# Performance work log

Hardware: AMD Instinct MI355X
Metric: run time of the kernel (lower is better)

Reference implementation:

```python
import jax, jax.numpy as jnp
import numpy as np

N, T, C, H, W = 4, 8, 512, 14, 14
HEADS = 8
D = C // HEADS            # 64 per-head dim
S = T * H * W             # 1568 sequence length
EPS = 1e-8
NEG = -2.0**32 + 1.0      # padding value used by the original module


def setup_inputs() -> dict:
    key = jax.random.key(0)
    ks = jax.random.split(key, 8)
    shp = (N, T, C, H, W)
    scale = 1.0 / np.sqrt(C)
    return {
        "queries": jax.random.normal(ks[0], shp, jnp.float32),
        "keys": jax.random.normal(ks[1], shp, jnp.float32),
        "values": jax.random.normal(ks[2], shp, jnp.float32),
        "Wq": jax.random.normal(ks[3], (C, C), jnp.float32) * scale,
        "bq": jnp.zeros((C,), jnp.float32),
        "Wk": jax.random.normal(ks[4], (C, C), jnp.float32) * scale,
        "bk": jnp.zeros((C,), jnp.float32),
        "Wv": jax.random.normal(ks[5], (C, C), jnp.float32) * scale,
        "bv": jnp.zeros((C,), jnp.float32),
        "gamma": jnp.ones((C,), jnp.float32),
        "beta": jnp.zeros((C,), jnp.float32),
    }


def _proj(x, Wt, b):
    # 1x1 Conv2d + ReLU over channel dim of (N, T, C, H, W)
    y = jnp.einsum('ntchw,oc->ntohw', x, Wt) + b[None, None, :, None, None]
    return jax.nn.relu(y)


def _flatten(x):
    # (N, T, C, H, W) -> (N, T*H*W, C)
    return x.transpose(0, 1, 3, 4, 2).reshape(N, S, C)


def _split_heads(x):
    # torch.cat(torch.chunk(x, HEADS, dim=2), dim=0): (N, S, C) -> (HEADS*N, S, D)
    return x.reshape(N, S, HEADS, D).transpose(2, 0, 1, 3).reshape(HEADS * N, S, D)


def reference(queries, keys, values, Wq, bq, Wk, bk, Wv, bv, gamma, beta):
    Qf = _flatten(_proj(queries, Wq, bq))
    Kf = _flatten(_proj(keys, Wk, bk))
    Vf = _flatten(_proj(values, Wv, bv))
    q_flat = _flatten(queries)   # residual + query mask source
    k_flat = _flatten(keys)      # key mask source

    Q_ = _split_heads(Qf)
    K_ = _split_heads(Kf)
    V_ = _split_heads(Vf)

    scores = jnp.einsum('bqd,bkd->bqk', Q_, K_) / jnp.sqrt(jnp.float32(D))

    # key padding mask: sign(|sum over C|), tiled over heads -> (HEADS*N, 1, S)
    key_mask = jnp.sign(jnp.abs(k_flat.sum(-1)))          # (N, S)
    km = jnp.tile(key_mask, (HEADS, 1))[:, None, :]
    scores = jnp.where(km == 0.0, NEG, scores)

    attn = jax.nn.softmax(scores, axis=-1)

    # query padding mask (multiplicative) -> (HEADS*N, S, 1)
    query_mask = jnp.sign(jnp.abs(q_flat.sum(-1)))        # (N, S)
    qm = jnp.tile(query_mask, (HEADS, 1))[:, :, None]
    attn = attn * qm

    out = jnp.einsum('bqk,bkd->bqd', attn, V_)
    # merge heads back: inverse of _split_heads
    out = out.reshape(HEADS, N, S, D).transpose(1, 2, 0, 3).reshape(N, S, C)

    out = out + q_flat  # residual

    # custom LayerNorm: torch .std() is unbiased (ddof=1)
    mean = out.mean(-1, keepdims=True)
    std = jnp.sqrt(out.var(-1, ddof=1, keepdims=True))
    out = gamma * (out - mean) / (std + EPS) + beta

    # reshape back to (N, T, C, H, W)
    return out.reshape(N, T, H, W, C).transpose(0, 1, 4, 2, 3)
```

## Files before the change

kernel.cpp:

```cpp
#include <hip/hip_runtime.h>
#include <math.h>

#define N_ 4
#define T_ 8
#define C_ 512
#define H_ 14
#define W_ 14
#define HEADS_ 8
#define D_ 64
#define HW_ 196
#define S_ 1568
#define P_TOT 6272
#define KMP_ 1600
#define NEGL_ (-1.0e38f)
#define EPS_ 1e-8f
#define QSC_ 0.18033688011112042f

typedef __attribute__((ext_vector_type(8))) short short8v;
typedef __attribute__((ext_vector_type(4))) float float4v;
typedef __attribute__((ext_vector_type(4))) unsigned short ushort4v;
typedef unsigned short ushort_t;

__device__ __forceinline__ ushort_t f2bf(float f) {
    union { float f; unsigned u; } a; a.f = f;
    unsigned r = (a.u + 0x7FFFu + ((a.u >> 16) & 1u)) >> 16;
    return (ushort_t)r;
}
__device__ __forceinline__ float bf2f(ushort_t u) {
    union { unsigned u; float f; } t; t.u = ((unsigned)u) << 16; return t.f;
}
__device__ __forceinline__ unsigned cvt_pk_bf16(float lo, float hi) {
    unsigned r;
    asm("v_cvt_pk_bf16_f32 %0, %1, %2" : "=v"(r) : "v"(lo), "v"(hi));
    return r;
}
__device__ __forceinline__ float exp2_fast(float x) {
    float r;
    asm("v_exp_f32 %0, %1" : "=v"(r) : "v"(x));
    return r;
}
__device__ __forceinline__ float max3f(float a, float b, float c) {
    float r;
    asm("v_max3_f32 %0, %1, %2, %3" : "=v"(r) : "v"(a), "v"(b), "v"(c));
    return r;
}
__device__ __forceinline__ float4v mfma16(short8v a, short8v b, float4v c) {
    return __builtin_amdgcn_mfma_f32_16x16x32_bf16(a, b, c, 0, 0, 0);
}
__device__ __forceinline__ void gload_lds16(const void* g, void* l) {
    __builtin_amdgcn_global_load_lds(
        (const __attribute__((address_space(1))) unsigned int*)g,
        (__attribute__((address_space(3))) unsigned int*)l,
        16, 0, 0);
}
__device__ __forceinline__ void gload_lds4(const void* g, void* l) {
    __builtin_amdgcn_global_load_lds(
        (const __attribute__((address_space(1))) unsigned int*)g,
        (__attribute__((address_space(3))) unsigned int*)l,
        4, 0, 0);
}

__global__ __launch_bounds__(256) void transpose_kernel(
    const float* __restrict__ q_in, const float* __restrict__ k_in,
    const float* __restrict__ v_in, ushort_t* __restrict__ qbf,
    ushort_t* __restrict__ kbf, ushort_t* __restrict__ vbf,
    const float* __restrict__ Wq, const float* __restrict__ Wk,
    const float* __restrict__ Wv, ushort_t* __restrict__ Wbf)
{
    __shared__ float Xs[64][197];
    const int z = blockIdx.z;
    const int nt = blockIdx.x;
    const int ct = blockIdx.y;
    const int tid = threadIdx.x;

    if (z == 3) {
        const int blk = nt * 8 + ct;
        #pragma unroll
        for (int i = 0; i < 3; ++i) {
            const int q = (blk * 3 + i) * 256 + tid;
            const int zi = q >> 16;
            const int qi = q & 65535;
            const float* src = (zi == 0) ? Wq : (zi == 1) ? Wk : Wv;
            const float4 v = *(const float4*)(src + qi * 4);
            ushort4v pk;
            pk[0] = f2bf(v.x); pk[1] = f2bf(v.y);
            pk[2] = f2bf(v.z); pk[3] = f2bf(v.w);
            *(ushort4v*)(Wbf + (long)zi * 262144 + qi * 4) = pk;
        }
        return;
    }

    const float* src = (z == 0) ? q_in : (z == 1) ? k_in : v_in;
    ushort_t* dst = (z == 0) ? qbf : (z == 1) ? kbf : vbf;

    const long gbase = ((long)nt * C_ + ct * 64) * HW_;
    #pragma unroll
    for (int i = 0; i < 13; ++i) {
        const int idx = i * 256 + tid;
        if (idx < 3136) {
            const int c = idx / 49;
            const int q4 = idx - c * 49;
            const float4 v = *(const float4*)(src + gbase + c * HW_ + q4 * 4);
            Xs[c][q4 * 4 + 0] = v.x;
            Xs[c][q4 * 4 + 1] = v.y;
            Xs[c][q4 * 4 + 2] = v.z;
            Xs[c][q4 * 4 + 3] = v.w;
        }
    }
    __syncthreads();
    const long pbase = (long)nt * HW_;
    const int c0 = (tid & 15) * 4;
    #pragma unroll
    for (int i = 0; i < 13; ++i) {
        const int idx = i * 256 + tid;
        if (idx < 3136) {
            const int hw = idx >> 4;
            ushort4v pk;
            #pragma unroll
            for (int e = 0; e < 4; ++e) pk[e] = f2bf(Xs[c0 + e][hw]);
            *(ushort4v*)(dst + (pbase + hw) * C_ + ct * 64 + c0) = pk;
        }
    }
}

__global__ __launch_bounds__(256) void mask_kernel(
    const ushort_t* __restrict__ qbf, const ushort_t* __restrict__ kbf,
    float* __restrict__ qm, float* __restrict__ km)
{
    const int tid = threadIdx.x;
    const int w = tid >> 6, lane = tid & 63;
    const int p = blockIdx.x * 4 + w;
    const short8v qv = *(const short8v*)(qbf + (long)p * C_ + lane * 8);
    const short8v kv = *(const short8v*)(kbf + (long)p * C_ + lane * 8);
    float sq = 0.f, sk = 0.f;
    #pragma unroll
    for (int j = 0; j < 8; ++j) {
        sq += bf2f(((const ushort_t*)&qv)[j]);
        sk += bf2f(((const ushort_t*)&kv)[j]);
    }
    #pragma unroll
    for (int off = 32; off > 0; off >>= 1) {
        sq += __shfl_xor(sq, off, 64);
        sk += __shfl_xor(sk, off, 64);
    }
    if (lane == 0) {
        const int n = p / S_, s = p - n * S_;
        qm[p] = (sq != 0.f) ? 1.f : 0.f;
        km[n * KMP_ + s] = (sk != 0.f) ? 0.f : NEGL_;
    }
    if (blockIdx.x == 0 && tid < 128) {
        const int nn = tid >> 5;
        const int ss = S_ + (tid & 31);
        km[nn * KMP_ + ss] = NEGL_;
    }
}

__global__ __launch_bounds__(256) void proj_all(
    const ushort_t* __restrict__ qbf, const ushort_t* __restrict__ kbf,
    const ushort_t* __restrict__ vbf, const ushort_t* __restrict__ Wbf,
    const float* __restrict__ bq, const float* __restrict__ bk,
    const float* __restrict__ bv,
    ushort_t* __restrict__ Qh, ushort_t* __restrict__ Kh,
    ushort_t* __restrict__ Vt)
{
    __shared__ char lds[49152];

    const int fid = blockIdx.x;
    const int xcd = fid & 7;
    const int iin = fid >> 3;
    const int v = xcd * 147 + iin;
    const int z = v / 392;
    const int rem = v - z * 392;
    const int ptile = rem >> 3;
    const int head = rem & 7;

    const ushort_t* Xbf = (z == 0) ? qbf : (z == 1) ? kbf : vbf;
    const ushort_t* Wz = Wbf + (long)z * 262144;
    const float* bias = (z == 0) ? bq : (z == 1) ? bk : bv;
    ushort_t* outp = (z == 0) ? Qh : (z == 1) ? Kh : Vt;
    const bool TR = (z == 2);
    const float osc = (z == 0) ? QSC_ : 1.0f;

    const int tid = threadIdx.x;
    const int w = tid >> 6, lane = tid & 63, lg = lane >> 4, lo = lane & 15;
    const int wr = w >> 1, wc = w & 1;
    const int p0 = ptile * 128;
    const int o0 = head * 64;

    const int wbase = (tid & 192) * 16;

    float4v acc[2][4];
    #pragma unroll
    for (int a = 0; a < 2; ++a)
        #pragma unroll
        for (int b = 0; b < 4; ++b) acc[a][b] = (float4v){0.f, 0.f, 0.f, 0.f};

    auto stage = [&](int buf, int k0) {
        char* Xl = lds + buf * 24576;
        char* Wl = Xl + 16384;
        #pragma unroll
        for (int i = 0; i < 4; ++i) {
            const int sl = tid + i * 256;
            const int row = sl >> 3, sir = sl & 7;
            const int c16 = sir ^ (row & 7);
            gload_lds16(Xbf + (long)(p0 + row) * C_ + k0 + c16 * 8,
                        Xl + i * 4096 + wbase);
        }
        #pragma unroll
        for (int i = 0; i < 2; ++i) {
            const int sl = tid + i * 256;
            const int row = sl >> 3, sir = sl & 7;
            const int c16 = sir ^ (row & 7);
            gload_lds16(Wz + (long)(o0 + row) * C_ + k0 + c16 * 8,
                        Wl + i * 4096 + wbase);
        }
    };

    stage(0, 0);
    #pragma unroll
    for (int kstep = 0; kstep < 8; ++kstep) {
        __syncthreads();
        if (kstep < 7) stage((kstep + 1) & 1, (kstep + 1) * 64);

        const char* Xl = lds + (kstep & 1) * 24576;
        const char* Wl = Xl + 16384;
        short8v wf[2][2], xf[4][2];
        #pragma unroll
        for (int a = 0; a < 2; ++a) {
            const int row = wc * 32 + a * 16 + lo;
            const int swr = (row & 7) << 4;
            #pragma unroll
            for (int ks = 0; ks < 2; ++ks) {
                const int base = row * 128 + ks * 64 + lg * 8;
                ((uint2*)&wf[a][ks])[0] = *(const uint2*)(Wl + (base ^ swr));
                ((uint2*)&wf[a][ks])[1] = *(const uint2*)(Wl + ((base + 32) ^ swr));
            }
        }
        #pragma unroll
        for (int b = 0; b < 4; ++b) {
            const int row = wr * 64 + b * 16 + lo;
            const int swr = (row & 7) << 4;
            #pragma unroll
            for (int ks = 0; ks < 2; ++ks) {
                const int base = row * 128 + ks * 64 + lg * 8;
                ((uint2*)&xf[b][ks])[0] = *(const uint2*)(Xl + (base ^ swr));
                ((uint2*)&xf[b][ks])[1] = *(const uint2*)(Xl + ((base + 32) ^ swr));
            }
        }
        __builtin_amdgcn_s_setprio(1);
        if (!TR) {
            #pragma unroll
            for (int ks = 0; ks < 2; ++ks)
                #pragma unroll
                for (int a = 0; a < 2; ++a)
                    #pragma unroll
                    for (int b = 0; b < 4; ++b)
                        acc[a][b] = mfma16(wf[a][ks], xf[b][ks], acc[a][b]);
        } else {
            #pragma unroll
            for (int ks = 0; ks < 2; ++ks)
                #pragma unroll
                for (int a = 0; a < 2; ++a)
                    #pragma unroll
                    for (int b = 0; b < 4; ++b)
                        acc[a][b] = mfma16(xf[b][ks], wf[a][ks], acc[a][b]);
        }
        __builtin_amdgcn_s_setprio(0);
    }

    if (!TR) {
        #pragma unroll
        for (int b = 0; b < 4; ++b) {
            const int p = p0 + wr * 64 + b * 16 + lo;
            const int nb = p / S_;
            const int s = p - nb * S_;
            #pragma unroll
            for (int a = 0; a < 2; ++a) {
                const int d0 = wc * 32 + a * 16 + lg * 4;
                const float4v bs = *(const float4v*)(bias + o0 + d0);
                ushort4v pk;
                #pragma unroll
                for (int e = 0; e < 4; ++e) {
                    float vv = acc[a][b][e] + bs[e];
                    vv = vv > 0.f ? vv : 0.f;
                    pk[e] = f2bf(vv * osc);
                }
                *(ushort4v*)(outp + ((long)(head * N_ + nb) * S_ + s) * D_ + d0) = pk;
            }
        }
    } else {
        #pragma unroll
        for (int a = 0; a < 2; ++a) {
            const int d = wc * 32 + a * 16 + lo;
            const float bsc = bias[o0 + d];
            #pragma unroll
            for (int b = 0; b < 4; ++b) {
                const int pb = p0 + wr * 64 + b * 16 + lg * 4;
                const int nb = pb / S_;
                const int s0 = pb - nb * S_;
                ushort4v pk;
                #pragma unroll
                for (int e = 0; e < 4; ++e) {
                    float vv = acc[a][b][e] + bsc;
                    vv = vv > 0.f ? vv : 0.f;
                    pk[e] = f2bf(vv);
                }
                *(ushort4v*)(outp + ((long)(head * N_ + nb) * D_ + d) * S_ + s0) = pk;
            }
        }
    }
}

__global__ __launch_bounds__(256) void attn_kernel(
    const ushort_t* __restrict__ Qh, const ushort_t* __restrict__ Kh,
    const ushort_t* __restrict__ Vt, const float* __restrict__ km,
    ushort_t* __restrict__ Pc, float* __restrict__ Ml)
{
    __shared__ char lds[16384 + 256];

    const int tid = threadIdx.x;
    const int lane = tid & 63;
    const int w = tid >> 6;
    const int lg = lane >> 4;
    const int lo = lane & 15;

    const int split = blockIdx.y;
    const int t1 = 7 + split * 6;
    const int t0 = split ? (1 + split * 6) : 0;

    const int fid = blockIdx.x;
    const int x = fid & 7;
    const int j = fid >> 3;
    const int b = x + 8 * (j / 25);
    const int q0 = (j % 25) * 64;
    const int n = b & (N_ - 1);

    char* Kl = lds;
    char* Vl = lds + 8192;
    const float* kms = (const float*)(lds + 16384);
    const int wbase = (tid & 192) * 16;

    const int qrow = q0 + w * 16 + lo;
    const int qcl = qrow < S_ ? qrow : S_ - 1;
    const ushort_t* qp = Qh + ((long)b * S_ + qcl) * D_ + lg * 4;
    short8v qf[2];
    #pragma unroll
    for (int ks = 0; ks < 2; ++ks) {
        ((uint2*)&qf[ks])[0] = *(const uint2*)(qp + ks * 32);
        ((uint2*)&qf[ks])[1] = *(const uint2*)(qp + ks * 32 + 16);
    }

    float4v acc[4];
    #pragma unroll
    for (int dt = 0; dt < 4; ++dt) acc[dt] = (float4v){0.f, 0.f, 0.f, 0.f};
    float m_run = -INFINITY, l_run = 0.f;

    auto stage = [&](int kb) {
        #pragma unroll
        for (int i = 0; i < 2; ++i) {
            const int s = i * 256 + tid;
            const int row = s >> 3;
            const int c16 = (s & 7) ^ (row & 7);
            int krow = kb + row; if (krow >= S_) krow = S_ - 1;
            gload_lds16(Kh + ((long)b * S_ + krow) * D_ + c16 * 8,
                        Kl + i * 4096 + wbase);
        }
        #pragma unroll
        for (int i = 0; i < 2; ++i) {
            const int s = i * 256 + tid;
            const int row = s >> 3;
            const int c16 = (s & 7) ^ (row & 7);
            int kc = kb + c16 * 8; if (kc > S_ - 8) kc = S_ - 8;
            gload_lds16(Vt + ((long)b * D_ + row) * S_ + kc,
                        Vl + i * 4096 + wbase);
        }
        if (w == 0)
            gload_lds4(km + (long)n * KMP_ + kb + lane, (void*)kms);
    };

    for (int t = t0; t < t1; ++t) {
        stage(t * 64);
        __syncthreads();

        float4v s[4];
        __builtin_amdgcn_s_setprio(1);
        #pragma unroll
        for (int kt = 0; kt < 4; ++kt) {
            s[kt] = (float4v){0.f, 0.f, 0.f, 0.f};
            #pragma unroll
            for (int ks = 0; ks < 2; ++ks) {
                const int row = kt * 16 + lo;
                const int base = row * 128 + ks * 64 + lg * 8;
                const int swr = (row & 7) << 4;
                short8v kf;
                ((uint2*)&kf)[0] = *(const uint2*)(Kl + (base ^ swr));
                ((uint2*)&kf)[1] = *(const uint2*)(Kl + ((base + 32) ^ swr));
                s[kt] = mfma16(kf, qf[ks], s[kt]);
            }
        }
        __builtin_amdgcn_s_setprio(0);

        float p[4][4];
        #pragma unroll
        for (int kt = 0; kt < 4; ++kt) {
            const float4v bv4 = *(const float4v*)&kms[kt * 16 + lg * 4];
            #pragma unroll
            for (int r = 0; r < 4; ++r) p[kt][r] = s[kt][r] + bv4[r];
        }
        const float m1 = max3f(p[0][0], p[0][1], p[0][2]);
        const float m2 = max3f(p[0][3], p[1][0], p[1][1]);
        const float m3 = max3f(p[1][2], p[1][3], p[2][0]);
        const float m4 = max3f(p[2][1], p[2][2], p[2][3]);
        const float m5 = max3f(p[3][0], p[3][1], p[3][2]);
        float mx = max3f(max3f(m1, m2, m3), m4, fmaxf(m5, p[3][3]));
        mx = fmaxf(mx, __shfl_xor(mx, 16, 64));
        mx = fmaxf(mx, __shfl_xor(mx, 32, 64));
        float mn;
        if (__all(mx <= m_run + 8.f)) {
            mn = m_run;
        } else {
            mn = fmaxf(m_run, mx);
            const float alpha = exp2_fast(m_run - mn);
            m_run = mn;
            l_run *= alpha;
            #pragma unroll
            for (int dt = 0; dt < 4; ++dt)
                #pragma unroll
                for (int r = 0; r < 4; ++r) acc[dt][r] *= alpha;
        }
        float rs4[4];
        #pragma unroll
        for (int kt = 0; kt < 4; ++kt) {
            #pragma unroll
            for (int r = 0; r < 4; ++r) p[kt][r] = exp2_fast(p[kt][r] - mn);
            rs4[kt] = (p[kt][0] + p[kt][1]) + (p[kt][2] + p[kt][3]);
        }
        l_run += (rs4[0] + rs4[1]) + (rs4[2] + rs4[3]);

        short8v pf[2];
        #pragma unroll
        for (int kt = 0; kt < 4; ++kt) {
            const unsigned w0 = cvt_pk_bf16(p[kt][0], p[kt][1]);
            const unsigned w1 = cvt_pk_bf16(p[kt][2], p[kt][3]);
            ((unsigned*)&pf[kt >> 1])[(kt & 1) * 2] = w0;
            ((unsigned*)&pf[kt >> 1])[(kt & 1) * 2 + 1] = w1;
        }

        __builtin_amdgcn_s_setprio(1);
        #pragma unroll
        for (int dt = 0; dt < 4; ++dt) {
            #pragma unroll
            for (int ks = 0; ks < 2; ++ks) {
                const int row = dt * 16 + lo;
                const int base = row * 128 + ks * 64 + lg * 8;
                const int swr = (row & 7) << 4;
                short8v vf;
                ((uint2*)&vf)[0] = *(const uint2*)(Vl + (base ^ swr));
                ((uint2*)&vf)[1] = *(const uint2*)(Vl + ((base + 32) ^ swr));
                acc[dt] = mfma16(vf, pf[ks], acc[dt]);
            }
        }
        __builtin_amdgcn_s_setprio(0);
        __syncthreads();
    }

    l_run += __shfl_xor(l_run, 16, 64);
    l_run += __shfl_xor(l_run, 32, 64);

    if (qrow < S_) {
        const long rbase = ((long)split * 32 + b) * S_ + qrow;
        if (lg == 0) {
            Ml[rbase * 2] = m_run;
            Ml[rbase * 2 + 1] = l_run;
        }
        ushort_t* P = Pc + rbase * 64;
        #pragma unroll
        for (int dt = 0; dt < 4; ++dt) {
            uint2 uu;
            uu.x = cvt_pk_bf16(acc[dt][0], acc[dt][1]);
            uu.y = cvt_pk_bf16(acc[dt][2], acc[dt][3]);
            *(uint2*)(P + dt * 16 + lg * 4) = uu;
        }
    }
}

__global__ __launch_bounds__(256) void combine_stats_kernel(
    const ushort_t* __restrict__ Pc, const float* __restrict__ Ml,
    const float* __restrict__ qm, const ushort_t* __restrict__ qbf,
    ushort_t* __restrict__ Om, float* __restrict__ stats)
{
    const int tid = threadIdx.x;
    const int wv = tid >> 6, lane = tid & 63;
    const long pos = (long)blockIdx.x * 4 + wv;
    const int n = (int)(pos / S_);
    const int q = (int)(pos - (long)n * S_);
    const int head = lane >> 3;
    const int d0 = (lane & 7) * 8;

    long rb[4];
    float mv[4], lv[4];
    float M = -INFINITY;
    #pragma unroll
    for (int s = 0; s < 4; ++s) {
        rb[s] = ((long)(s * 32 + head * 4 + n) * S_ + q);
        const float2 ml = *(const float2*)(Ml + rb[s] * 2);
        mv[s] = ml.x; lv[s] = ml.y;
        M = fmaxf(M, ml.x);
    }
    float L = 0.f;
    float o[8] = {0.f, 0.f, 0.f, 0.f, 0.f, 0.f, 0.f, 0.f};
    #pragma unroll
    for (int s = 0; s < 4; ++s) {
        const float wgt = exp2_fast(mv[s] - M);
        L = fmaf(lv[s], wgt, L);
        const ushort4v a0 = *(const ushort4v*)(Pc + rb[s] * 64 + d0);
        const ushort4v a1 = *(const ushort4v*)(Pc + rb[s] * 64 + d0 + 4);
        #pragma unroll
        for (int e = 0; e < 4; ++e) {
            o[e] = fmaf(bf2f(a0[e]), wgt, o[e]);
            o[4 + e] = fmaf(bf2f(a1[e]), wgt, o[4 + e]);
        }
    }
    L = fmaxf(L, 1e-20f);
    const float scale = qm[pos] / L;
    const short8v qv = *(const short8v*)(qbf + pos * C_ + lane * 8);
    ushort4v ov0, ov1;
    float sum = 0.f, ssq = 0.f;
    #pragma unroll
    for (int e = 0; e < 8; ++e) {
        const ushort_t ob = f2bf(o[e] * scale);
        if (e < 4) ov0[e] = ob; else ov1[e - 4] = ob;
        const float v = bf2f(ob) + bf2f(((const ushort_t*)&qv)[e]);
        sum += v; ssq += v * v;
    }
    #pragma unroll
    for (int off = 32; off > 0; off >>= 1) {
        sum += __shfl_xor(sum, off, 64);
        ssq += __shfl_xor(ssq, off, 64);
    }
    *(ushort4v*)(Om + pos * C_ + lane * 8) = ov0;
    *(ushort4v*)(Om + pos * C_ + lane * 8 + 4) = ov1;
    if (lane == 0) {
        const float mean = sum * (1.f / 512.f);
        float var = (ssq - sum * mean) * (1.f / 511.f);
        var = var > 0.f ? var : 0.f;
        stats[pos * 2] = mean;
        stats[pos * 2 + 1] = 1.f / (sqrtf(var) + EPS_);
    }
}

__global__ __launch_bounds__(256) void ln_write_kernel(
    const ushort_t* __restrict__ Om, const ushort_t* __restrict__ qbf,
    const float* __restrict__ stats, const float* __restrict__ gamma,
    const float* __restrict__ beta, float* __restrict__ out)
{
    __shared__ float Tl[64][197];
    const int nt = blockIdx.x;
    const int ct = blockIdx.y;
    const int tid = threadIdx.x;

    const int c0 = (tid & 15) * 4;
    float g[4], bb[4];
    #pragma unroll
    for (int e = 0; e < 4; ++e) {
        g[e] = gamma[ct * 64 + c0 + e];
        bb[e] = beta[ct * 64 + c0 + e];
    }

    #pragma unroll
    for (int i = 0; i < 13; ++i) {
        const int idx = i * 256 + tid;
        if (idx < 3136) {
            const int hw = idx >> 4;
            const long p = (long)nt * HW_ + hw;
            const float mean = stats[p * 2];
            const float inv = stats[p * 2 + 1];
            const ushort4v ov = *(const ushort4v*)(Om + p * C_ + ct * 64 + c0);
            const ushort4v qv = *(const ushort4v*)(qbf + p * C_ + ct * 64 + c0);
            #pragma unroll
            for (int e = 0; e < 4; ++e) {
                const float xv = bf2f(ov[e]) + bf2f(qv[e]);
                Tl[c0 + e][hw] = g[e] * (xv - mean) * inv + bb[e];
            }
        }
    }
    __syncthreads();
    const long obase = ((long)nt * C_ + ct * 64) * HW_;
    #pragma unroll
    for (int i = 0; i < 13; ++i) {
        const int idx = i * 256 + tid;
        if (idx < 3136) {
            const int c = idx / 49;
            const int q4 = idx - c * 49;
            float4 v;
            v.x = Tl[c][q4 * 4 + 0];
            v.y = Tl[c][q4 * 4 + 1];
            v.z = Tl[c][q4 * 4 + 2];
            v.w = Tl[c][q4 * 4 + 3];
            *(float4*)(out + obase + c * HW_ + q4 * 4) = v;
        }
    }
}

extern "C" void kernel_launch(void* const* d_in, const int* in_sizes, int n_in,
                              void* d_out, int out_size, void* d_ws, size_t ws_size,
                              hipStream_t stream) {
    const float* q_in  = (const float*)d_in[0];
    const float* k_in  = (const float*)d_in[1];
    const float* v_in  = (const float*)d_in[2];
    const float* Wq    = (const float*)d_in[3];
    const float* bq    = (const float*)d_in[4];
    const float* Wk    = (const float*)d_in[5];
    const float* bk    = (const float*)d_in[6];
    const float* Wv    = (const float*)d_in[7];
    const float* bv    = (const float*)d_in[8];
    const float* gamma = (const float*)d_in[9];
    const float* beta  = (const float*)d_in[10];
    float* out = (float*)d_out;

    const size_t PC = (size_t)P_TOT * C_;
    ushort_t* qbf = (ushort_t*)d_ws;
    ushort_t* kbf = qbf + PC;
    ushort_t* vbf = kbf + PC;
    ushort_t* Wbf = vbf + PC;
    ushort_t* Qh  = Wbf + 3 * (size_t)C_ * C_;
    ushort_t* Kh  = Qh + PC;
    ushort_t* Vt  = Kh + PC;
    ushort_t* Om  = Vt + PC;
    ushort_t* Pc  = Om + PC;
    float* Ml    = (float*)(Pc + 4L * 32 * S_ * 64);
    float* stats = Ml + 4L * 32 * S_ * 2;
    float* qm    = stats + 2 * P_TOT;
    float* km    = qm + P_TOT;

    transpose_kernel<<<dim3(32, 8, 4), 256, 0, stream>>>(
        q_in, k_in, v_in, qbf, kbf, vbf, Wq, Wk, Wv, Wbf);
    mask_kernel<<<P_TOT / 4, 256, 0, stream>>>(qbf, kbf, qm, km);
    proj_all<<<1176, 256, 0, stream>>>(qbf, kbf, vbf, Wbf, bq, bk, bv, Qh, Kh, Vt);
    attn_kernel<<<dim3(800, 4), 256, 0, stream>>>(Qh, Kh, Vt, km, Pc, Ml);
    combine_stats_kernel<<<P_TOT / 4, 256, 0, stream>>>(Pc, Ml, qm, qbf, Om, stats);
    ln_write_kernel<<<dim3(32, 8), 256, 0, stream>>>(Om, qbf, stats, gamma, beta, out);
}
```

Measured before the change: 101.5 us.

## Process two 64-row query tiles per attention block to reuse staged K/V

Each attention workgroup now handles 128 query rows, as two groups of 64, instead of 64. Each K/V tile staged in LDS and each K/V fragment read from LDS feeds MFMAs for both groups. This halves global K/V staging traffic and LDS reads per query row, and the grid shrinks from 800 to 416 blocks per split. In exchange, register pressure roughly doubles for the accumulators and scores, which may lower occupancy, and the smaller grid gives less parallelism on a large GPU. The last tile also carries more padded rows.

```diff
diff --git a/kernel.cpp b/kernel.cpp
--- a/kernel.cpp
+++ b/kernel.cpp
@@ -331,8 +331,8 @@
     const int fid = blockIdx.x;
     const int x = fid & 7;
     const int j = fid >> 3;
-    const int b = x + 8 * (j / 25);
-    const int q0 = (j % 25) * 64;
+    const int b = x + 8 * (j / 13);
+    const int q0 = (j % 13) * 128;
     const int n = b & (N_ - 1);
 
     char* Kl = lds;
@@ -340,20 +340,27 @@
     const float* kms = (const float*)(lds + 16384);
     const int wbase = (tid & 192) * 16;
 
-    const int qrow = q0 + w * 16 + lo;
-    const int qcl = qrow < S_ ? qrow : S_ - 1;
-    const ushort_t* qp = Qh + ((long)b * S_ + qcl) * D_ + lg * 4;
-    short8v qf[2];
-    #pragma unroll
-    for (int ks = 0; ks < 2; ++ks) {
-        ((uint2*)&qf[ks])[0] = *(const uint2*)(qp + ks * 32);
-        ((uint2*)&qf[ks])[1] = *(const uint2*)(qp + ks * 32 + 16);
-    }
-
-    float4v acc[4];
-    #pragma unroll
-    for (int dt = 0; dt < 4; ++dt) acc[dt] = (float4v){0.f, 0.f, 0.f, 0.f};
-    float m_run = -INFINITY, l_run = 0.f;
+    int qrow[2];
+    short8v qf[2][2];
+    #pragma unroll
+    for (int g = 0; g < 2; ++g) {
+        qrow[g] = q0 + g * 64 + w * 16 + lo;
+        const int qcl = qrow[g] < S_ ? qrow[g] : S_ - 1;
+        const ushort_t* qp = Qh + ((long)b * S_ + qcl) * D_ + lg * 4;
+        #pragma unroll
+        for (int ks = 0; ks < 2; ++ks) {
+            ((uint2*)&qf[g][ks])[0] = *(const uint2*)(qp + ks * 32);
+            ((uint2*)&qf[g][ks])[1] = *(const uint2*)(qp + ks * 32 + 16);
+        }
+    }
+
+    float4v acc[2][4];
+    #pragma unroll
+    for (int g = 0; g < 2; ++g)
+        #pragma unroll
+        for (int dt = 0; dt < 4; ++dt) acc[g][dt] = (float4v){0.f, 0.f, 0.f, 0.f};
+    float m_run[2] = {-INFINITY, -INFINITY};
+    float l_run[2] = {0.f, 0.f};
 
     auto stage = [&](int kb) {
         #pragma unroll
@@ -382,104 +389,114 @@
         stage(t * 64);
         __syncthreads();
 
-        float4v s[4];
+        float4v s[2][4];
         __builtin_amdgcn_s_setprio(1);
         #pragma unroll
         for (int kt = 0; kt < 4; ++kt) {
-            s[kt] = (float4v){0.f, 0.f, 0.f, 0.f};
+            #pragma unroll
+            for (int g = 0; g < 2; ++g) s[g][kt] = (float4v){0.f, 0.f, 0.f, 0.f};
+            const int row = kt * 16 + lo;
+            const int base = row * 128 + lg * 8;
+            const int swr = (row & 7) << 4;
             #pragma unroll
             for (int ks = 0; ks < 2; ++ks) {
-                const int row = kt * 16 + lo;
-                const int base = row * 128 + ks * 64 + lg * 8;
-                const int swr = (row & 7) << 4;
                 short8v kf;
-                ((uint2*)&kf)[0] = *(const uint2*)(Kl + (base ^ swr));
-                ((uint2*)&kf)[1] = *(const uint2*)(Kl + ((base + 32) ^ swr));
-                s[kt] = mfma16(kf, qf[ks], s[kt]);
+                ((uint2*)&kf)[0] = *(const uint2*)(Kl + ((base + ks * 64) ^ swr));
+                ((uint2*)&kf)[1] = *(const uint2*)(Kl + ((base + ks * 64 + 32) ^ swr));
+                #pragma unroll
+                for (int g = 0; g < 2; ++g)
+                    s[g][kt] = mfma16(kf, qf[g][ks], s[g][kt]);
             }
         }
         __builtin_amdgcn_s_setprio(0);
 
-        float p[4][4];
-        #pragma unroll
-        for (int kt = 0; kt < 4; ++kt) {
-            const float4v bv4 = *(const float4v*)&kms[kt * 16 + lg * 4];
-            #pragma unroll
-            for (int r = 0; r < 4; ++r) p[kt][r] = s[kt][r] + bv4[r];
-        }
-        const float m1 = max3f(p[0][0], p[0][1], p[0][2]);
-        const float m2 = max3f(p[0][3], p[1][0], p[1][1]);
-        const float m3 = max3f(p[1][2], p[1][3], p[2][0]);
-        const float m4 = max3f(p[2][1], p[2][2], p[2][3]);
-        const float m5 = max3f(p[3][0], p[3][1], p[3][2]);
-        float mx = max3f(max3f(m1, m2, m3), m4, fmaxf(m5, p[3][3]));
-        mx = fmaxf(mx, __shfl_xor(mx, 16, 64));
-        mx = fmaxf(mx, __shfl_xor(mx, 32, 64));
-        float mn;
-        if (__all(mx <= m_run + 8.f)) {
-            mn = m_run;
-        } else {
-            mn = fmaxf(m_run, mx);
-            const float alpha = exp2_fast(m_run - mn);
-            m_run = mn;
-            l_run *= alpha;
-            #pragma unroll
-            for (int dt = 0; dt < 4; ++dt)
-                #pragma unroll
-                for (int r = 0; r < 4; ++r) acc[dt][r] *= alpha;
-        }
-        float rs4[4];
-        #pragma unroll
-        for (int kt = 0; kt < 4; ++kt) {
-            #pragma unroll
-            for (int r = 0; r < 4; ++r) p[kt][r] = exp2_fast(p[kt][r] - mn);
-            rs4[kt] = (p[kt][0] + p[kt][1]) + (p[kt][2] + p[kt][3]);
-        }
-        l_run += (rs4[0] + rs4[1]) + (rs4[2] + rs4[3]);
-
-        short8v pf[2];
-        #pragma unroll
-        for (int kt = 0; kt < 4; ++kt) {
-            const unsigned w0 = cvt_pk_bf16(p[kt][0], p[kt][1]);
-            const unsigned w1 = cvt_pk_bf16(p[kt][2], p[kt][3]);
-            ((unsigned*)&pf[kt >> 1])[(kt & 1) * 2] = w0;
-            ((unsigned*)&pf[kt >> 1])[(kt & 1) * 2 + 1] = w1;
+        short8v pf[2][2];
+        #pragma unroll
+        for (int g = 0; g < 2; ++g) {
+            float p[4][4];
+            #pragma unroll
+            for (int kt = 0; kt < 4; ++kt) {
+                const float4v bv4 = *(const float4v*)&kms[kt * 16 + lg * 4];
+                #pragma unroll
+                for (int r = 0; r < 4; ++r) p[kt][r] = s[g][kt][r] + bv4[r];
+            }
+            const float m1 = max3f(p[0][0], p[0][1], p[0][2]);
+            const float m2 = max3f(p[0][3], p[1][0], p[1][1]);
+            const float m3 = max3f(p[1][2], p[1][3], p[2][0]);
+            const float m4 = max3f(p[2][1], p[2][2], p[2][3]);
+            const float m5 = max3f(p[3][0], p[3][1], p[3][2]);
+            float mx = max3f(max3f(m1, m2, m3), m4, fmaxf(m5, p[3][3]));
+            mx = fmaxf(mx, __shfl_xor(mx, 16, 64));
+            mx = fmaxf(mx, __shfl_xor(mx, 32, 64));
+            float mn;
+            if (__all(mx <= m_run[g] + 8.f)) {
+                mn = m_run[g];
+            } else {
+                mn = fmaxf(m_run[g], mx);
+                const float alpha = exp2_fast(m_run[g] - mn);
+                m_run[g] = mn;
+                l_run[g] *= alpha;
+                #pragma unroll
+                for (int dt = 0; dt < 4; ++dt)
+                    #pragma unroll
+                    for (int r = 0; r < 4; ++r) acc[g][dt][r] *= alpha;
+            }
+            float rs4[4];
+            #pragma unroll
+            for (int kt = 0; kt < 4; ++kt) {
+                #pragma unroll
+                for (int r = 0; r < 4; ++r) p[kt][r] = exp2_fast(p[kt][r] - mn);
+                rs4[kt] = (p[kt][0] + p[kt][1]) + (p[kt][2] + p[kt][3]);
+            }
+            l_run[g] += (rs4[0] + rs4[1]) + (rs4[2] + rs4[3]);
+
+            #pragma unroll
+            for (int kt = 0; kt < 4; ++kt) {
+                const unsigned w0 = cvt_pk_bf16(p[kt][0], p[kt][1]);
+                const unsigned w1 = cvt_pk_bf16(p[kt][2], p[kt][3]);
+                ((unsigned*)&pf[g][kt >> 1])[(kt & 1) * 2] = w0;
+                ((unsigned*)&pf[g][kt >> 1])[(kt & 1) * 2 + 1] = w1;
+            }
         }
 
         __builtin_amdgcn_s_setprio(1);
         #pragma unroll
         for (int dt = 0; dt < 4; ++dt) {
+            const int row = dt * 16 + lo;
+            const int base = row * 128 + lg * 8;
+            const int swr = (row & 7) << 4;
             #pragma unroll
             for (int ks = 0; ks < 2; ++ks) {
-                const int row = dt * 16 + lo;
-                const int base = row * 128 + ks * 64 + lg * 8;
-                const int swr = (row & 7) << 4;
                 short8v vf;
-                ((uint2*)&vf)[0] = *(const uint2*)(Vl + (base ^ swr));
-                ((uint2*)&vf)[1] = *(const uint2*)(Vl + ((base + 32) ^ swr));
-                acc[dt] = mfma16(vf, pf[ks], acc[dt]);
+                ((uint2*)&vf)[0] = *(const uint2*)(Vl + ((base + ks * 64) ^ swr));
+                ((uint2*)&vf)[1] = *(const uint2*)(Vl + ((base + ks * 64 + 32) ^ swr));
+                #pragma unroll
+                for (int g = 0; g < 2; ++g)
+                    acc[g][dt] = mfma16(vf, pf[g][ks], acc[g][dt]);
             }
         }
         __builtin_amdgcn_s_setprio(0);
         __syncthreads();
     }
 
-    l_run += __shfl_xor(l_run, 16, 64);
-    l_run += __shfl_xor(l_run, 32, 64);
-
-    if (qrow < S_) {
-        const long rbase = ((long)split * 32 + b) * S_ + qrow;
-        if (lg == 0) {
-            Ml[rbase * 2] = m_run;
-            Ml[rbase * 2 + 1] = l_run;
-        }
-        ushort_t* P = Pc + rbase * 64;
-        #pragma unroll
-        for (int dt = 0; dt < 4; ++dt) {
-            uint2 uu;
-            uu.x = cvt_pk_bf16(acc[dt][0], acc[dt][1]);
-            uu.y = cvt_pk_bf16(acc[dt][2], acc[dt][3]);
-            *(uint2*)(P + dt * 16 + lg * 4) = uu;
+    #pragma unroll
+    for (int g = 0; g < 2; ++g) {
+        l_run[g] += __shfl_xor(l_run[g], 16, 64);
+        l_run[g] += __shfl_xor(l_run[g], 32, 64);
+        if (qrow[g] < S_) {
+            const long rbase = ((long)split * 32 + b) * S_ + qrow[g];
+            if (lg == 0) {
+                Ml[rbase * 2] = m_run[g];
+                Ml[rbase * 2 + 1] = l_run[g];
+            }
+            ushort_t* P = Pc + rbase * 64;
+            #pragma unroll
+            for (int dt = 0; dt < 4; ++dt) {
+                uint2 uu;
+                uu.x = cvt_pk_bf16(acc[g][dt][0], acc[g][dt][1]);
+                uu.y = cvt_pk_bf16(acc[g][dt][2], acc[g][dt][3]);
+                *(uint2*)(P + dt * 16 + lg * 4) = uu;
+            }
         }
     }
 }
@@ -637,7 +654,7 @@
         q_in, k_in, v_in, qbf, kbf, vbf, Wq, Wk, Wv, Wbf);
     mask_kernel<<<P_TOT / 4, 256, 0, stream>>>(qbf, kbf, qm, km);
     proj_all<<<1176, 256, 0, stream>>>(qbf, kbf, vbf, Wbf, bq, bk, bv, Qh, Kh, Vt);
-    attn_kernel<<<dim3(800, 4), 256, 0, stream>>>(Qh, Kh, Vt, km, Pc, Ml);
+    attn_kernel<<<dim3(416, 4), 256, 0, stream>>>(Qh, Kh, Vt, km, Pc, Ml);
     combine_stats_kernel<<<P_TOT / 4, 256, 0, stream>>>(Pc, Ml, qm, qbf, Om, stats);
     ln_write_kernel<<<dim3(32, 8), 256, 0, stream>>>(Om, qbf, stats, gamma, beta, out);
 }
```

Result: slower. 106.4 us (+4.9%).
